# Performance work log

Hardware: AMD Instinct MI355X
Metric: run time of the kernel (lower is better)

## Reference

```python
import jax, jax.numpy as jnp
import numpy as np

# --- SLAYER params (nmnistNet.yaml) ---
THETA = 10.0
TS = 1.0
TAU_REF = 1.0
SCALE_REF = 2.0
T_SAMPLE = 300
B = 8

def _alpha_kernel(tau, mult, t_sample, ts, eps=0.01):
    vals = []
    t = 0.0
    while t < t_sample:
        v = mult * t / tau * np.exp(1.0 - t / tau)
        if abs(v) < eps and t > tau:
            break
        vals.append(v)
        t += ts
    return np.asarray(vals, np.float32)

# refractory kernel: alpha kernel with mult = -scaleRef*theta (slayer._calculateRefKernel)
REF_KERNEL = _alpha_kernel(TAU_REF, -SCALE_REF * THETA, T_SAMPLE, TS)
NREF = REF_KERNEL.shape[0]  # 11 for these params; REF_KERNEL[0] == 0


def spike(u):
    """slayerCuda.getSpikes: per-neuron sequential threshold recurrence over time.
    u: [..., T] membrane potential. On spike at t, REF_KERNEL is accumulated
    into u[t:t+NREF]; spike amplitude is 1/Ts."""
    uT = jnp.moveaxis(u, -1, 0)  # [T, ...]
    refk = jnp.asarray(REF_KERNEL[1:]).reshape((NREF - 1,) + (1,) * (u.ndim - 1))
    buf0 = jnp.zeros((NREF - 1,) + uT.shape[1:], u.dtype)  # pending refractory

    def step(buf, u_t):
        u_mod = u_t + buf[0]
        ev = (u_mod >= THETA).astype(u.dtype)
        buf = jnp.concatenate([buf[1:], jnp.zeros_like(buf[:1])], axis=0) + ev[None] * refk
        return buf, ev / TS

    _, s = jax.lax.scan(step, buf0, uT)
    return jnp.moveaxis(s, 0, -1)


def conv2d_t(x, w, pad):
    """slayer.conv: Conv3d with kernel (k,k,1) == per-timestep 2D conv.
    x: [B,C,H,W,T], w: [O,I,kh,kw]."""
    b, c, h, wd, t = x.shape
    xb = jnp.moveaxis(x, -1, 1).reshape(b * t, c, h, wd)
    y = jax.lax.conv_general_dilated(xb, w, (1, 1), [(pad, pad), (pad, pad)],
                                     dimension_numbers=('NCHW', 'OIHW', 'NCHW'))
    o, ho, wo = y.shape[1], y.shape[2], y.shape[3]
    return jnp.moveaxis(y.reshape(b, t, o, ho, wo), 1, -1)


def sum_pool2(x):
    """slayer.pool(2): fixed-weight (1.1*theta) 2x2/stride-2 sum over H,W per channel."""
    y = jax.lax.reduce_window(x, 0.0, jax.lax.add, (1, 1, 2, 2, 1), (1, 1, 2, 2, 1), 'VALID')
    return 1.1 * THETA * y


def setup_inputs():
    key = jax.random.key(0)
    k0, k1, k2, k3, k4 = jax.random.split(key, 5)
    spikeInput = (jax.random.uniform(k0, (B, 2, 34, 34, T_SAMPLE)) < 0.1).astype(jnp.float32) / TS
    # conv weights: kaiming-uniform bound * 100 (the __init__ scales conv weights by 100)
    w1 = jax.random.uniform(k1, (16, 2, 5, 5), minval=-14.1, maxval=14.1, dtype=jnp.float32)
    w2 = jax.random.uniform(k2, (32, 16, 3, 3), minval=-8.3, maxval=8.3, dtype=jnp.float32)
    w3 = jax.random.uniform(k3, (64, 32, 3, 3), minval=-5.9, maxval=5.9, dtype=jnp.float32)
    wfc = jax.random.uniform(k4, (10, 64, 8, 8), minval=-0.5, maxval=0.5, dtype=jnp.float32)
    return {"spikeInput": spikeInput, "w1": w1, "w2": w2, "w3": w3, "wfc": wfc}


def reference(spikeInput, w1, w2, w3, wfc):
    s1 = spike(conv2d_t(spikeInput, w1, 1))  # [B,16,32,32,T]
    s2 = spike(sum_pool2(s1))                # [B,16,16,16,T]
    s3 = spike(conv2d_t(s2, w2, 1))          # [B,32,16,16,T]
    s4 = spike(sum_pool2(s3))                # [B,32,8,8,T]
    s5 = spike(conv2d_t(s4, w3, 1))          # [B,64,8,8,T]
    # dense((8,8,64),10): Conv3d(64,10,(8,8,1)) == full-spatial contraction
    u = jnp.einsum('bchwt,ochw->bot', s5, wfc)[:, :, None, None, :]
    return spike(u)                          # [B,10,1,1,T]
```

## Files before the change

kernel.cpp:

```cpp
#include <hip/hip_runtime.h>
#include <hip/hip_bf16.h>
#include <cmath>

#define T_SAMPLE 300
#define NCHUNK 75

typedef __attribute__((ext_vector_type(8))) short short8;
typedef __attribute__((ext_vector_type(4))) float f32x4;

struct RefK { float v[10]; };

__device__ __forceinline__ unsigned char spike_step(float u, float* buf, const RefK& rk) {
    const float um = u + buf[0];
    const bool fire = um >= 10.0f;
    const float ev = fire ? 1.0f : 0.0f;
#pragma unroll
    for (int r = 0; r < 9; ++r) buf[r] = fmaf(ev, rk.v[r], buf[r + 1]);
    buf[9] = ev * rk.v[9];
    return fire ? (unsigned char)1 : (unsigned char)0;
}

__device__ __forceinline__ short8 bytes_to_bf16x8(uint2 w8) {
    union { uint4 u; short8 s8; } cv;
    cv.u.x = (w8.x & 0xFFu) * 0x3F80u | ((((w8.x >> 8) & 0xFFu) * 0x3F80u) << 16);
    cv.u.y = ((w8.x >> 16) & 0xFFu) * 0x3F80u | ((((w8.x >> 24) & 0xFFu) * 0x3F80u) << 16);
    cv.u.z = (w8.y & 0xFFu) * 0x3F80u | ((((w8.y >> 8) & 0xFFu) * 0x3F80u) << 16);
    cv.u.w = ((w8.y >> 16) & 0xFFu) * 0x3F80u | ((((w8.y >> 24) & 0xFFu) * 0x3F80u) << 16);
    return cv.s8;
}

__device__ __forceinline__ unsigned short bf16_split_sel(float w, int s) {
    __hip_bfloat16 hb = __float2bfloat16(w);
    const float hf = __bfloat162float(hb);
    __hip_bfloat16 mb = __float2bfloat16(w - hf);
    const float mf = __bfloat162float(mb);
    __hip_bfloat16 lb = __float2bfloat16(w - hf - mf);
    __hip_bfloat16 sel = (s == 0) ? hb : ((s == 1) ? mb : lb);
    return *(unsigned short*)&sel;
}

__global__ __launch_bounds__(256) void transpose_in_k(
    const float* __restrict__ In, unsigned int* __restrict__ X)
{
    __shared__ unsigned int lds[16 * NCHUNK];
    const int blk = blockIdx.x;
    const int tn = threadIdx.x >> 4;
    const int tq = threadIdx.x & 15;
    const size_t n = (size_t)blk * 16 + tn;
#pragma unroll
    for (int p = 0; p < 5; ++p) {
        const int ch = p * 16 + tq;
        if (ch < NCHUNK) {
            const float4 v = *(const float4*)(In + n * T_SAMPLE + ch * 4);
            unsigned int u = (v.x != 0.f ? 1u : 0u) | (v.y != 0.f ? 0x100u : 0u) |
                             (v.z != 0.f ? 0x10000u : 0u) | (v.w != 0.f ? 0x1000000u : 0u);
            lds[tn * NCHUNK + ch] = u;
        }
    }
    __syncthreads();
    for (int idx = threadIdx.x; idx < 16 * NCHUNK; idx += 256) {
        const int ch = idx >> 4, t2 = idx & 15;
        X[(size_t)ch * 18496 + blk * 16 + t2] = lds[t2 * NCHUNK + ch];
    }
}

__global__ __launch_bounds__(256) void prep_w1_k(
    const float* __restrict__ w1, unsigned short* __restrict__ Wr1)
{
    const int g = blockIdx.x * 256 + threadIdx.x;
    const int j = g & 7;
    const int lane = (g >> 3) & 63;
    const int ks = (g >> 9) & 3;
    const int s = g >> 11;
    const int q = lane >> 4;
    const int oc = lane & 15;
    const int kg = ks * 32 + q * 8 + j;
    const int slot = kg >> 2, c = kg & 1;
    const int dy = slot / 6, dx = slot % 6;
    const float w = (dy < 5 && dx < 5) ? w1[((oc * 2 + c) * 5 + dy) * 5 + dx] * 0.5f : 0.f;
    Wr1[g] = bf16_split_sel(w, s);
}

__global__ __launch_bounds__(256) void prep_w3_k(
    const float* __restrict__ w3, unsigned short* __restrict__ Wr)
{
    const int g = blockIdx.x * 256 + threadIdx.x;
    const int j = g & 7;
    const int lane = (g >> 3) & 63;
    const int mt = (g >> 9) & 3;
    const int rest = g >> 11;
    const int ks = rest % 9;
    const int s = rest / 9;
    const int oc = mt * 16 + (lane & 15);
    const int ic = (lane >> 4) * 8 + j;
    Wr[g] = bf16_split_sel(w3[(oc * 32 + ic) * 9 + ks], s);
}

__global__ __launch_bounds__(256) void prep_w2_k(
    const float* __restrict__ w2, unsigned short* __restrict__ Wr2)
{
    const int g = blockIdx.x * 256 + threadIdx.x;
    const int j = g & 7;
    const int lane = (g >> 3) & 63;
    const int mt = (g >> 9) & 1;
    const int rest = g >> 10;
    const int kp = rest % 5;
    const int s = rest / 5;
    const int q = lane >> 4;
    const int oc = mt * 16 + (lane & 15);
    const int tap = kp * 2 + (q >> 1);
    const int ic = (q & 1) * 8 + j;
    const float w = (tap <= 8) ? w2[(oc * 16 + ic) * 9 + tap] : 0.f;
    Wr2[g] = bf16_split_sel(w, s);
}

__device__ __forceinline__ void c1_mfma_chunk(
    const unsigned int* __restrict__ tb, const int* offA, const int* offB,
    const short8* Af, f32x4* acc)
{
    unsigned int vA[4][4], vB[4][4];
#pragma unroll
    for (int ks = 0; ks < 4; ++ks)
#pragma unroll
        for (int t = 0; t < 4; ++t) {
            vA[ks][t] = tb[t * 72 + offA[ks]];
            vB[ks][t] = tb[t * 72 + offB[ks]];
        }

#pragma unroll
    for (int t = 0; t < 4; ++t) acc[t] = (f32x4){0.f, 0.f, 0.f, 0.f};
#pragma unroll
    for (int ks = 0; ks < 4; ++ks)
#pragma unroll
        for (int t = 0; t < 4; ++t) {
            union { uint4 u; short8 s8; } cv;
            cv.u.x = vA[ks][t]; cv.u.y = vA[ks][t];
            cv.u.z = vB[ks][t]; cv.u.w = vB[ks][t];
#pragma unroll
            for (int s = 0; s < 3; ++s)
                acc[t] = __builtin_amdgcn_mfma_f32_16x16x32_bf16(
                    Af[s * 4 + ks], cv.s8, acc[t], 0, 0, 0);
        }
}

__global__ __launch_bounds__(256) void conv1ps_k(
    const unsigned int* __restrict__ X, const unsigned short* __restrict__ Wr1,
    uchar4* __restrict__ S1, RefK rk)
{
    __shared__ unsigned int tab[15 * 288];
    __shared__ __align__(16) float4 Ulds[15 * 256];
    const int pg = blockIdx.x;
    const int b = blockIdx.y;
    const int ty = pg >> 2, tx = pg & 3;
    const int tid = threadIdx.x;
    const int wv = tid >> 6, lane = tid & 63;
    const int q = lane >> 4, n = lane & 15;
    const int py0 = n >> 3, px0 = n & 7;

    short8 Af[12];
#pragma unroll
    for (int s = 0; s < 3; ++s)
#pragma unroll
        for (int ks = 0; ks < 4; ++ks)
            Af[s * 4 + ks] = *(const short8*)(Wr1 + (((s * 4 + ks) * 64 + lane) * 8));

    int offA[4], offB[4];
#pragma unroll
    for (int ks = 0; ks < 4; ++ks) {
        const int sA = ks * 8 + q * 2, sB = sA + 1;
        const int dyA = sA / 6, dxA = sA - dyA * 6;
        const int dyB = sB / 6, dxB = sB - dyB * 6;
        offA[ks] = min(py0 + dyA, 5) * 12 + min(px0 + dxA, 11);
        offB[ks] = min(py0 + dyB, 5) * 12 + min(px0 + dxB, 11);
    }

    int lidx[5];
    int gof[5];
#pragma unroll
    for (int i = 0; i < 5; ++i) {
        const int e = i * 256 + tid;
        if (e < 1080) {
            const int chl = e / 72, site = e - chl * 72;
            const int r = site / 12, cc = site - r * 12;
            const int gy = ty * 2 - 1 + r, gx = tx * 8 - 1 + cc;
            lidx[i] = chl * 288 + site;
            gof[i] = (((unsigned)gy < 34u) && ((unsigned)gx < 34u))
                   ? (chl * 18496 + (b * 2) * 1156 + gy * 34 + gx) : -1;
        } else { lidx[i] = -1; gof[i] = -1; }
    }

    unsigned int w0[5], w1[5];
#pragma unroll
    for (int i = 0; i < 5; ++i) {
        if (gof[i] >= 0) { w0[i] = X[gof[i]]; w1[i] = X[gof[i] + 1156]; }
        else { w0[i] = 0u; w1[i] = 0u; }
    }

    float buf[10];
#pragma unroll
    for (int r = 0; r < 10; ++r) buf[r] = 0.f;
    const int s_oc = tid >> 4, s_n = tid & 15;
    const int nb0 = (b * 16 + s_oc) * 1024 + (ty * 2 + (s_n >> 3)) * 32 + tx * 8 + (s_n & 7);

    for (int w = 0; w < 5; ++w) {
#pragma unroll
        for (int i = 0; i < 5; ++i) {
            if (lidx[i] >= 0) {
#pragma unroll
                for (int t = 0; t < 4; ++t)
                    tab[lidx[i] + t * 72] =
                        ((w0[i] >> (8 * t)) & 0xFFu) * 0x3F80u
                        | ((((w1[i] >> (8 * t)) & 0xFFu) * 0x3F80u) << 16);
            }
        }
        __syncthreads();

        for (int k = wv; k < 15; k += 4) {
            f32x4 acc[4];
            c1_mfma_chunk(tab + k * 288, offA, offB, Af, acc);
#pragma unroll
            for (int rr = 0; rr < 4; ++rr)
                Ulds[k * 256 + (q * 4 + rr) * 16 + n] =
                    make_float4(acc[0][rr], acc[1][rr], acc[2][rr], acc[3][rr]);
        }
        __syncthreads();

        if (w < 4) {
            const unsigned int* Xs = X + (size_t)(w + 1) * (15 * 18496);
#pragma unroll
            for (int i = 0; i < 5; ++i) {
                if (gof[i] >= 0) { w0[i] = Xs[gof[i]]; w1[i] = Xs[gof[i] + 1156]; }
            }
        }

        for (int k = 0; k < 15; ++k) {
            const float4 u = Ulds[k * 256 + tid];
            uchar4 o;
            o.x = spike_step(u.x, buf, rk);
            o.y = spike_step(u.y, buf, rk);
            o.z = spike_step(u.z, buf, rk);
            o.w = spike_step(u.w, buf, rk);
            S1[(size_t)(w * 15 + k) * 131072 + nb0] = o;
        }
    }
}

__global__ __launch_bounds__(256) void conv2_mfma_k(
    const unsigned int* __restrict__ s2u, const unsigned short* __restrict__ Wr2,
    float4* __restrict__ U, int b0, int nbl)
{
    __shared__ __align__(16) unsigned char pad[4 * 18 * 18 * 16];
    const int tc = blockIdx.x;
    const int bl = blockIdx.z;
    const int b = b0 + bl;
    const int tid = threadIdx.x;
    const int wv = tid >> 6, lane = tid & 63;
    const int q = lane >> 4, n = lane & 15;
    const int PLANE_U = nbl * 8192;

    unsigned int* lp = (unsigned int*)pad;
    for (int i = tid; i < 5184; i += 256) lp[i] = 0u;
    __syncthreads();
    const unsigned int* sb = s2u + (size_t)tc * 32768 + b * 4096;
    for (int e = tid; e < 4096; e += 256) {
        const unsigned int v = sb[e];
        const int c = e >> 8, pix = e & 255;
        const int base = (((pix >> 4) + 1) * 18 + ((pix & 15) + 1)) * 16 + c;
        pad[base]         = (unsigned char)(v & 0xFFu);
        pad[5184 + base]  = (unsigned char)((v >> 8) & 0xFFu);
        pad[10368 + base] = (unsigned char)((v >> 16) & 0xFFu);
        pad[15552 + base] = (unsigned char)(v >> 24);
    }
    __syncthreads();

    for (int i = 0; i < 4; ++i) {
        const int r = wv * 4 + i;
        f32x4 acc[2][4];
#pragma unroll
        for (int mt = 0; mt < 2; ++mt)
#pragma unroll
            for (int t = 0; t < 4; ++t) acc[mt][t] = (f32x4){0.f, 0.f, 0.f, 0.f};

        for (int kp = 0; kp < 5; ++kp) {
            short8 Af[6];
#pragma unroll
            for (int s = 0; s < 3; ++s)
#pragma unroll
                for (int mt = 0; mt < 2; ++mt)
                    Af[s * 2 + mt] = *(const short8*)(Wr2 + ((((s * 5 + kp) * 2 + mt) * 64 + lane) * 8));
            int tap = kp * 2 + (q >> 1);
            if (tap > 8) tap = 8;
            const int dy = tap / 3, dx = tap % 3;
#pragma unroll
            for (int t = 0; t < 4; ++t) {
                const int off = ((t * 18 + r + dy) * 18 + (n + dx)) * 16 + (q & 1) * 8;
                const short8 Bf = bytes_to_bf16x8(*(const uint2*)(pad + off));
#pragma unroll
                for (int s = 0; s < 3; ++s)
#pragma unroll
                    for (int mt = 0; mt < 2; ++mt)
                        acc[mt][t] = __builtin_amdgcn_mfma_f32_16x16x32_bf16(
                            Af[s * 2 + mt], Bf, acc[mt][t], 0, 0, 0);
            }
        }

        const size_t ub = (size_t)tc * PLANE_U;
#pragma unroll
        for (int mt = 0; mt < 2; ++mt)
#pragma unroll
            for (int rr = 0; rr < 4; ++rr) {
                const int oc = mt * 16 + q * 4 + rr;
                const int nb = (bl * 32 + oc) * 256 + r * 16 + n;
                U[ub + nb] = make_float4(acc[mt][0][rr], acc[mt][1][rr], acc[mt][2][rr], acc[mt][3][rr]);
            }
    }
}

__global__ __launch_bounds__(256) void conv3_mfma_k(
    const unsigned int* __restrict__ s4u, const unsigned short* __restrict__ Wr,
    float4* __restrict__ U)
{
    __shared__ __align__(16) unsigned char pad[12800];
    const int tc = blockIdx.x;
    const int bl = blockIdx.z;
    const int tid = threadIdx.x;
    const int wv = tid >> 6, lane = tid & 63;
    const int q = lane >> 4, n = lane & 15;

    unsigned int* lp = (unsigned int*)pad;
    for (int i = tid; i < 3200; i += 256) lp[i] = 0u;
    __syncthreads();
    const unsigned int* sb = s4u + (size_t)tc * 16384 + bl * 2048;
    for (int e = tid; e < 2048; e += 256) {
        const unsigned int v = sb[e];
        const int c = e >> 6, pix = e & 63;
        const int base = (((pix >> 3) + 1) * 10 + ((pix & 7) + 1)) * 32 + c;
        pad[base]        = (unsigned char)(v & 0xFFu);
        pad[3200 + base] = (unsigned char)((v >> 8) & 0xFFu);
        pad[6400 + base] = (unsigned char)((v >> 16) & 0xFFu);
        pad[9600 + base] = (unsigned char)(v >> 24);
    }
    __syncthreads();

    const int pixel = wv * 16 + n;
    const int py0 = pixel >> 3, px0 = pixel & 7;

    f32x4 acc[4][4];
#pragma unroll
    for (int mt = 0; mt < 4; ++mt)
#pragma unroll
        for (int t = 0; t < 4; ++t) acc[mt][t] = (f32x4){0.f, 0.f, 0.f, 0.f};

    for (int ks = 0; ks < 9; ++ks) {
        const int dy = ks / 3, dx = ks % 3;
        short8 Af[12];
#pragma unroll
        for (int s = 0; s < 3; ++s)
#pragma unroll
            for (int mt = 0; mt < 4; ++mt)
                Af[s * 4 + mt] = *(const short8*)(Wr + ((((s * 9 + ks) * 4 + mt) * 64 + lane) * 8));
#pragma unroll
        for (int t = 0; t < 4; ++t) {
            const int off = ((t * 10 + py0 + dy) * 10 + (px0 + dx)) * 32 + q * 8;
            const short8 Bf = bytes_to_bf16x8(*(const uint2*)(pad + off));
#pragma unroll
            for (int s = 0; s < 3; ++s)
#pragma unroll
                for (int mt = 0; mt < 4; ++mt)
                    acc[mt][t] = __builtin_amdgcn_mfma_f32_16x16x32_bf16(
                        Af[s * 4 + mt], Bf, acc[mt][t], 0, 0, 0);
        }
    }

    const size_t ub = (size_t)tc * 32768 + (size_t)bl * 4096;
#pragma unroll
    for (int mt = 0; mt < 4; ++mt)
#pragma unroll
        for (int r = 0; r < 4; ++r) {
            const int oc = mt * 16 + q * 4 + r;
            const int nb = oc * 64 + wv * 16 + n;
            U[ub + nb] = make_float4(acc[mt][0][r], acc[mt][1][r], acc[mt][2][r], acc[mt][3][r]);
        }
}

__device__ __forceinline__ void spike_body(
    const float4* __restrict__ U, uchar4* __restrict__ S,
    int nneur, int sstride, int soff, const RefK& rk)
{
    const int n = blockIdx.x * 64 + threadIdx.x;
    const float4* up = U + n;
    uchar4* sp = S + soff + n;
    float buf[10];
#pragma unroll
    for (int r = 0; r < 10; ++r) buf[r] = 0.f;

    float4 ring[8];
#pragma unroll
    for (int r = 0; r < 8; ++r) ring[r] = up[(size_t)r * nneur];

#pragma unroll 8
    for (int ch = 0; ch < 72; ++ch) {
        const float4 cur = ring[ch & 7];
        const int pf = (ch + 8 < NCHUNK) ? ch + 8 : NCHUNK - 1;
        ring[ch & 7] = up[(size_t)pf * nneur];
        uchar4 o;
        o.x = spike_step(cur.x, buf, rk);
        o.y = spike_step(cur.y, buf, rk);
        o.z = spike_step(cur.z, buf, rk);
        o.w = spike_step(cur.w, buf, rk);
        sp[(size_t)ch * sstride] = o;
    }
#pragma unroll
    for (int ch = 72; ch < NCHUNK; ++ch) {
        const float4 cur = ring[ch & 7];
        uchar4 o;
        o.x = spike_step(cur.x, buf, rk);
        o.y = spike_step(cur.y, buf, rk);
        o.z = spike_step(cur.z, buf, rk);
        o.w = spike_step(cur.w, buf, rk);
        sp[(size_t)ch * sstride] = o;
    }
}

__global__ __launch_bounds__(64) void spike2_k(
    const float4* U, uchar4* S, int nneur, int sstride, int soff, RefK rk)
{ spike_body(U, S, nneur, sstride, soff, rk); }

__global__ __launch_bounds__(64) void spike3_k(
    const float4* U, uchar4* S, int nneur, int sstride, int soff, RefK rk)
{ spike_body(U, S, nneur, sstride, soff, rk); }

__device__ __forceinline__ int bsum4(uint2 r0, uint2 r1, int k) {
    return (int)((r0.x >> (8 * k)) & 0xffu) + (int)((r0.y >> (8 * k)) & 0xffu)
         + (int)((r1.x >> (8 * k)) & 0xffu) + (int)((r1.y >> (8 * k)) & 0xffu);
}

template <int C, int H, int W>
__device__ __forceinline__ void pool_body(
    const uchar4* __restrict__ Sin, uchar4* __restrict__ Sout, const RefK& rk)
{
    constexpr int H2 = H / 2, W2 = W / 2;
    constexpr int SIN = 8 * C * H * W;
    constexpr int SOUT = 8 * C * H2 * W2;
    const int n = blockIdx.x * 64 + threadIdx.x;
    const int x = n % W2;
    const int y = (n / W2) % H2;
    const int c = (n / (W2 * H2)) % C;
    const int b = n / (W2 * H2 * C);
    const int base = (((b * C + c) * H + 2 * y) * W + 2 * x);
    uchar4* q = Sout + n;

    float buf[10];
#pragma unroll
    for (int r = 0; r < 10; ++r) buf[r] = 0.f;

    uint2 r0[8], r1[8];
#pragma unroll
    for (int r = 0; r < 8; ++r) {
        r0[r] = *(const uint2*)(Sin + (size_t)r * SIN + base);
        r1[r] = *(const uint2*)(Sin + (size_t)r * SIN + base + W);
    }

#pragma unroll 8
    for (int ch = 0; ch < 72; ++ch) {
        const uint2 a0 = r0[ch & 7], a1 = r1[ch & 7];
        const int pf = (ch + 8 < NCHUNK) ? ch + 8 : NCHUNK - 1;
        r0[ch & 7] = *(const uint2*)(Sin + (size_t)pf * SIN + base);
        r1[ch & 7] = *(const uint2*)(Sin + (size_t)pf * SIN + base + W);
        uchar4 o;
        o.x = spike_step(11.0f * (float)bsum4(a0, a1, 0), buf, rk);
        o.y = spike_step(11.0f * (float)bsum4(a0, a1, 1), buf, rk);
        o.z = spike_step(11.0f * (float)bsum4(a0, a1, 2), buf, rk);
        o.w = spike_step(11.0f * (float)bsum4(a0, a1, 3), buf, rk);
        q[(size_t)ch * SOUT] = o;
    }
#pragma unroll
    for (int ch = 72; ch < NCHUNK; ++ch) {
        const uint2 a0 = r0[ch & 7], a1 = r1[ch & 7];
        uchar4 o;
        o.x = spike_step(11.0f * (float)bsum4(a0, a1, 0), buf, rk);
        o.y = spike_step(11.0f * (float)bsum4(a0, a1, 1), buf, rk);
        o.z = spike_step(11.0f * (float)bsum4(a0, a1, 2), buf, rk);
        o.w = spike_step(11.0f * (float)bsum4(a0, a1, 3), buf, rk);
        q[(size_t)ch * SOUT] = o;
    }
}

__global__ __launch_bounds__(64) void pool2_k(
    const uchar4* Sin, uchar4* Sout, RefK rk) { pool_body<16, 32, 32>(Sin, Sout, rk); }
__global__ __launch_bounds__(64) void pool4_k(
    const uchar4* Sin, uchar4* Sout, RefK rk) { pool_body<32, 16, 16>(Sin, Sout, rk); }

__global__ __launch_bounds__(64) void dense_k(
    const uchar4* __restrict__ S5, const float* __restrict__ WFC,
    float4* __restrict__ U6)
{
    const int tc = blockIdx.x, o = blockIdx.y, b = blockIdx.z;
    const int lane = threadIdx.x;
    float a0 = 0.f, a1 = 0.f, a2 = 0.f, a3 = 0.f;
    const uchar4* sb = S5 + (size_t)tc * 32768 + b * 4096;
    const float* wb = WFC + o * 4096;
    for (int i = 0; i < 64; ++i) {
        const int site = i * 64 + lane;
        const uchar4 s = sb[site];
        const float w = wb[site];
        a0 = fmaf(w, (float)s.x, a0);
        a1 = fmaf(w, (float)s.y, a1);
        a2 = fmaf(w, (float)s.z, a2);
        a3 = fmaf(w, (float)s.w, a3);
    }
#pragma unroll
    for (int m = 1; m < 64; m <<= 1) {
        a0 += __shfl_xor(a0, m, 64);
        a1 += __shfl_xor(a1, m, 64);
        a2 += __shfl_xor(a2, m, 64);
        a3 += __shfl_xor(a3, m, 64);
    }
    if (lane == 0)
        U6[(size_t)tc * 80 + b * 10 + o] = make_float4(a0, a1, a2, a3);
}

__global__ __launch_bounds__(128) void spike6_k(
    const float4* __restrict__ U6, float* __restrict__ Out, RefK rk)
{
    const int n = threadIdx.x;
    if (n >= 80) return;
    const float4* up = U6 + n;
    float* op = Out + (size_t)n * T_SAMPLE;
    float buf[10];
#pragma unroll
    for (int r = 0; r < 10; ++r) buf[r] = 0.f;

    float4 ring[8];
#pragma unroll
    for (int r = 0; r < 8; ++r) ring[r] = up[(size_t)r * 80];

#pragma unroll 8
    for (int ch = 0; ch < 72; ++ch) {
        const float4 cur = ring[ch & 7];
        const int pf = (ch + 8 < NCHUNK) ? ch + 8 : NCHUNK - 1;
        ring[ch & 7] = up[(size_t)pf * 80];
        float4 o;
        o.x = (float)spike_step(cur.x, buf, rk);
        o.y = (float)spike_step(cur.y, buf, rk);
        o.z = (float)spike_step(cur.z, buf, rk);
        o.w = (float)spike_step(cur.w, buf, rk);
        *(float4*)(op + ch * 4) = o;
    }
#pragma unroll
    for (int ch = 72; ch < NCHUNK; ++ch) {
        const float4 cur = ring[ch & 7];
        float4 o;
        o.x = (float)spike_step(cur.x, buf, rk);
        o.y = (float)spike_step(cur.y, buf, rk);
        o.z = (float)spike_step(cur.z, buf, rk);
        o.w = (float)spike_step(cur.w, buf, rk);
        *(float4*)(op + ch * 4) = o;
    }
}

extern "C" void kernel_launch(void* const* d_in, const int* in_sizes, int n_in,
                              void* d_out, int out_size, void* d_ws, size_t ws_size,
                              hipStream_t stream)
{
    const float* spikeIn = (const float*)d_in[0];
    const float* w1 = (const float*)d_in[1];
    const float* w2 = (const float*)d_in[2];
    const float* w3 = (const float*)d_in[3];
    const float* wfc = (const float*)d_in[4];
    float* out = (float*)d_out;

    RefK rk;
    for (int t = 1; t <= 10; ++t)
        rk.v[t - 1] = (float)(-20.0 * (double)t * std::exp(1.0 - (double)t));

    const size_t A_BYTES = 39321600;
    const size_t B_BYTES = 9830400;
    const size_t U6_BYTES = 96000;
    const size_t U_BIG = 78643200, U_SMALL = 39321600;
    const size_t TAIL = A_BYTES + B_BYTES + U6_BYTES;
    const bool big = ws_size >= U_BIG + TAIL;
    const size_t U_BYTES = big ? U_BIG : U_SMALL;

    char* ws = (char*)d_ws;
    float4* U = (float4*)ws;
    uchar4* A = (uchar4*)(ws + U_BYTES);
    uchar4* Bb = (uchar4*)(ws + U_BYTES + A_BYTES);
    float4* U6 = (float4*)(ws + U_BYTES + A_BYTES + B_BYTES);
    unsigned short* Wr = (unsigned short*)(ws + U_BYTES + 20971520);
    unsigned short* Wr2 = (unsigned short*)(ws + U_BYTES + 20971520 + 131072);
    unsigned short* Wr1 = (unsigned short*)(ws + U_BYTES + A_BYTES + 5570560);

    uchar4* X = Bb;
    uchar4* s1 = A;
    uchar4* s2 = Bb;
    uchar4* s3 = A;
    uchar4* s4 = Bb;
    uchar4* s5 = A;

    transpose_in_k<<<18496 / 16, 256, 0, stream>>>(spikeIn, (unsigned int*)X);
    prep_w1_k<<<24, 256, 0, stream>>>(w1, Wr1);

    {
        dim3 g1(64, 8);
        conv1ps_k<<<g1, 256, 0, stream>>>((const unsigned int*)X, Wr1, s1, rk);
    }
    pool2_k<<<32768 / 64, 64, 0, stream>>>(s1, s2, rk);
    prep_w2_k<<<60, 256, 0, stream>>>(w2, Wr2);
    prep_w3_k<<<216, 256, 0, stream>>>(w3, Wr);
    const int nbl2 = big ? 8 : 4;
    for (int b0 = 0; b0 < 8; b0 += nbl2) {
        dim3 g2(NCHUNK, 1, nbl2);
        conv2_mfma_k<<<g2, 256, 0, stream>>>((const unsigned int*)s2, Wr2, U, b0, nbl2);
        const int nn = nbl2 * 8192;
        spike2_k<<<nn / 64, 64, 0, stream>>>(U, s3, nn, 65536, b0 * 8192, rk);
    }
    pool4_k<<<16384 / 64, 64, 0, stream>>>(s3, s4, rk);
    {
        dim3 g3(NCHUNK, 1, 8);
        conv3_mfma_k<<<g3, 256, 0, stream>>>((const unsigned int*)s4, Wr, U);
        spike3_k<<<32768 / 64, 64, 0, stream>>>(U, s5, 32768, 32768, 0, rk);
    }
    dim3 g6(NCHUNK, 10, 8);
    dense_k<<<g6, 64, 0, stream>>>(s5, wfc, U6);
    spike6_k<<<1, 128, 0, stream>>>(U6, out, rk);
}
```

Measured before the change: 259.3 us.

## Warp-specialize conv1 into producer/consumer waves and fuse dense outputs per block

Conv1 now launches 512-thread blocks. Four waves compute MFMA convolution chunks into double-buffered LDS while the other four run the sequential spike recurrence on the previous chunk, so compute and the serial threshold scan overlap. The input loads for the next window are also prefetched into a second tab buffer. Separately, dense_k computes all 10 outputs in one block instead of one block per output, reusing each spike load across outputs at the cost of many more registers.

```diff
diff --git a/kernel.cpp b/kernel.cpp
--- a/kernel.cpp
+++ b/kernel.cpp
@@ -143,104 +143,130 @@
         }
 }
 
-__global__ __launch_bounds__(256) void conv1ps_k(
+__global__ __launch_bounds__(512, 4) void conv1pc_k(
     const unsigned int* __restrict__ X, const unsigned short* __restrict__ Wr1,
     uchar4* __restrict__ S1, RefK rk)
 {
-    __shared__ unsigned int tab[15 * 288];
-    __shared__ __align__(16) float4 Ulds[15 * 256];
+    __shared__ unsigned int tab[2][5 * 288];
+    __shared__ __align__(16) float4 Ulds[2][5 * 256];
     const int pg = blockIdx.x;
     const int b = blockIdx.y;
     const int ty = pg >> 2, tx = pg & 3;
     const int tid = threadIdx.x;
     const int wv = tid >> 6, lane = tid & 63;
+    const bool isConv = (wv >= 4);
     const int q = lane >> 4, n = lane & 15;
     const int py0 = n >> 3, px0 = n & 7;
 
     short8 Af[12];
-#pragma unroll
-    for (int s = 0; s < 3; ++s)
-#pragma unroll
-        for (int ks = 0; ks < 4; ++ks)
-            Af[s * 4 + ks] = *(const short8*)(Wr1 + (((s * 4 + ks) * 64 + lane) * 8));
-
     int offA[4], offB[4];
-#pragma unroll
-    for (int ks = 0; ks < 4; ++ks) {
-        const int sA = ks * 8 + q * 2, sB = sA + 1;
-        const int dyA = sA / 6, dxA = sA - dyA * 6;
-        const int dyB = sB / 6, dxB = sB - dyB * 6;
-        offA[ks] = min(py0 + dyA, 5) * 12 + min(px0 + dxA, 11);
-        offB[ks] = min(py0 + dyB, 5) * 12 + min(px0 + dxB, 11);
-    }
-
-    int lidx[5];
-    int gof[5];
-#pragma unroll
-    for (int i = 0; i < 5; ++i) {
-        const int e = i * 256 + tid;
-        if (e < 1080) {
-            const int chl = e / 72, site = e - chl * 72;
-            const int r = site / 12, cc = site - r * 12;
-            const int gy = ty * 2 - 1 + r, gx = tx * 8 - 1 + cc;
-            lidx[i] = chl * 288 + site;
-            gof[i] = (((unsigned)gy < 34u) && ((unsigned)gx < 34u))
-                   ? (chl * 18496 + (b * 2) * 1156 + gy * 34 + gx) : -1;
-        } else { lidx[i] = -1; gof[i] = -1; }
-    }
-
-    unsigned int w0[5], w1[5];
-#pragma unroll
-    for (int i = 0; i < 5; ++i) {
-        if (gof[i] >= 0) { w0[i] = X[gof[i]]; w1[i] = X[gof[i] + 1156]; }
-        else { w0[i] = 0u; w1[i] = 0u; }
-    }
-
-    float buf[10];
-#pragma unroll
-    for (int r = 0; r < 10; ++r) buf[r] = 0.f;
-    const int s_oc = tid >> 4, s_n = tid & 15;
-    const int nb0 = (b * 16 + s_oc) * 1024 + (ty * 2 + (s_n >> 3)) * 32 + tx * 8 + (s_n & 7);
-
-    for (int w = 0; w < 5; ++w) {
-#pragma unroll
-        for (int i = 0; i < 5; ++i) {
+    int lidx[2], gof[2];
+    unsigned int w0[2], w1[2];
+    if (isConv) {
+#pragma unroll
+        for (int s = 0; s < 3; ++s)
+#pragma unroll
+            for (int ks = 0; ks < 4; ++ks)
+                Af[s * 4 + ks] = *(const short8*)(Wr1 + (((s * 4 + ks) * 64 + lane) * 8));
+#pragma unroll
+        for (int ks = 0; ks < 4; ++ks) {
+            const int sA = ks * 8 + q * 2, sB = sA + 1;
+            const int dyA = sA / 6, dxA = sA - dyA * 6;
+            const int dyB = sB / 6, dxB = sB - dyB * 6;
+            offA[ks] = min(py0 + dyA, 5) * 12 + min(px0 + dxA, 11);
+            offB[ks] = min(py0 + dyB, 5) * 12 + min(px0 + dxB, 11);
+        }
+        const int tid2 = tid - 256;
+#pragma unroll
+        for (int i = 0; i < 2; ++i) {
+            const int e = i * 256 + tid2;
+            if (e < 360) {
+                const int chl = e / 72, site = e - chl * 72;
+                const int r = site / 12, cc = site - r * 12;
+                const int gy = ty * 2 - 1 + r, gx = tx * 8 - 1 + cc;
+                lidx[i] = chl * 288 + site;
+                gof[i] = (((unsigned)gy < 34u) && ((unsigned)gx < 34u))
+                       ? (chl * 18496 + (b * 2) * 1156 + gy * 34 + gx) : -1;
+            } else { lidx[i] = -1; gof[i] = -1; }
+        }
+#pragma unroll
+        for (int i = 0; i < 2; ++i) {
+            if (gof[i] >= 0) { w0[i] = X[gof[i]]; w1[i] = X[gof[i] + 1156]; }
+            else { w0[i] = 0u; w1[i] = 0u; }
+        }
+#pragma unroll
+        for (int i = 0; i < 2; ++i) {
             if (lidx[i] >= 0) {
 #pragma unroll
                 for (int t = 0; t < 4; ++t)
-                    tab[lidx[i] + t * 72] =
+                    tab[0][lidx[i] + t * 72] =
                         ((w0[i] >> (8 * t)) & 0xFFu) * 0x3F80u
                         | ((((w1[i] >> (8 * t)) & 0xFFu) * 0x3F80u) << 16);
             }
         }
+    }
+
+    float buf[10];
+#pragma unroll
+    for (int r = 0; r < 10; ++r) buf[r] = 0.f;
+    const int s_oc = (tid & 255) >> 4, s_n = tid & 15;
+    const int nb0 = (b * 16 + s_oc) * 1024 + (ty * 2 + (s_n >> 3)) * 32 + tx * 8 + (s_n & 7);
+
+    __syncthreads();
+
+    for (int w = 0; w < 15; ++w) {
+        const int cb = w & 1;
+        if (isConv) {
+            if (w < 14) {
+                const unsigned int* Xs = X + (size_t)(w + 1) * (5 * 18496);
+#pragma unroll
+                for (int i = 0; i < 2; ++i) {
+                    if (gof[i] >= 0) { w0[i] = Xs[gof[i]]; w1[i] = Xs[gof[i] + 1156]; }
+                }
+            }
+            for (int k = wv - 4; k < 5; k += 4) {
+                f32x4 acc[4];
+                c1_mfma_chunk(&tab[cb][k * 288], offA, offB, Af, acc);
+#pragma unroll
+                for (int rr = 0; rr < 4; ++rr)
+                    Ulds[cb][k * 256 + (q * 4 + rr) * 16 + n] =
+                        make_float4(acc[0][rr], acc[1][rr], acc[2][rr], acc[3][rr]);
+            }
+            if (w < 14) {
+#pragma unroll
+                for (int i = 0; i < 2; ++i) {
+                    if (lidx[i] >= 0) {
+#pragma unroll
+                        for (int t = 0; t < 4; ++t)
+                            tab[cb ^ 1][lidx[i] + t * 72] =
+                                ((w0[i] >> (8 * t)) & 0xFFu) * 0x3F80u
+                                | ((((w1[i] >> (8 * t)) & 0xFFu) * 0x3F80u) << 16);
+                    }
+                }
+            }
+        } else if (w > 0) {
+            const int pb = (w - 1) & 1;
+            for (int k = 0; k < 5; ++k) {
+                const float4 u = Ulds[pb][k * 256 + tid];
+                uchar4 o;
+                o.x = spike_step(u.x, buf, rk);
+                o.y = spike_step(u.y, buf, rk);
+                o.z = spike_step(u.z, buf, rk);
+                o.w = spike_step(u.w, buf, rk);
+                S1[(size_t)((w - 1) * 5 + k) * 131072 + nb0] = o;
+            }
+        }
         __syncthreads();
-
-        for (int k = wv; k < 15; k += 4) {
-            f32x4 acc[4];
-            c1_mfma_chunk(tab + k * 288, offA, offB, Af, acc);
-#pragma unroll
-            for (int rr = 0; rr < 4; ++rr)
-                Ulds[k * 256 + (q * 4 + rr) * 16 + n] =
-                    make_float4(acc[0][rr], acc[1][rr], acc[2][rr], acc[3][rr]);
-        }
-        __syncthreads();
-
-        if (w < 4) {
-            const unsigned int* Xs = X + (size_t)(w + 1) * (15 * 18496);
-#pragma unroll
-            for (int i = 0; i < 5; ++i) {
-                if (gof[i] >= 0) { w0[i] = Xs[gof[i]]; w1[i] = Xs[gof[i] + 1156]; }
-            }
-        }
-
-        for (int k = 0; k < 15; ++k) {
-            const float4 u = Ulds[k * 256 + tid];
+    }
+    if (!isConv) {
+        for (int k = 0; k < 5; ++k) {
+            const float4 u = Ulds[0][k * 256 + tid];
             uchar4 o;
             o.x = spike_step(u.x, buf, rk);
             o.y = spike_step(u.y, buf, rk);
             o.z = spike_step(u.z, buf, rk);
             o.w = spike_step(u.w, buf, rk);
-            S1[(size_t)(w * 15 + k) * 131072 + nb0] = o;
+            S1[(size_t)(70 + k) * 131072 + nb0] = o;
         }
     }
 }
@@ -495,29 +521,45 @@
     const uchar4* __restrict__ S5, const float* __restrict__ WFC,
     float4* __restrict__ U6)
 {
-    const int tc = blockIdx.x, o = blockIdx.y, b = blockIdx.z;
+    const int tc = blockIdx.x, b = blockIdx.z;
     const int lane = threadIdx.x;
-    float a0 = 0.f, a1 = 0.f, a2 = 0.f, a3 = 0.f;
+    float a[10][4];
+#pragma unroll
+    for (int o = 0; o < 10; ++o)
+#pragma unroll
+        for (int j = 0; j < 4; ++j) a[o][j] = 0.f;
+
     const uchar4* sb = S5 + (size_t)tc * 32768 + b * 4096;
-    const float* wb = WFC + o * 4096;
+#pragma unroll 4
     for (int i = 0; i < 64; ++i) {
         const int site = i * 64 + lane;
         const uchar4 s = sb[site];
-        const float w = wb[site];
-        a0 = fmaf(w, (float)s.x, a0);
-        a1 = fmaf(w, (float)s.y, a1);
-        a2 = fmaf(w, (float)s.z, a2);
-        a3 = fmaf(w, (float)s.w, a3);
-    }
-#pragma unroll
-    for (int m = 1; m < 64; m <<= 1) {
-        a0 += __shfl_xor(a0, m, 64);
-        a1 += __shfl_xor(a1, m, 64);
-        a2 += __shfl_xor(a2, m, 64);
-        a3 += __shfl_xor(a3, m, 64);
-    }
-    if (lane == 0)
-        U6[(size_t)tc * 80 + b * 10 + o] = make_float4(a0, a1, a2, a3);
+        const float sx = (float)s.x, sy = (float)s.y;
+        const float sz = (float)s.z, sw = (float)s.w;
+#pragma unroll
+        for (int o = 0; o < 10; ++o) {
+            const float w = WFC[o * 4096 + site];
+            a[o][0] = fmaf(w, sx, a[o][0]);
+            a[o][1] = fmaf(w, sy, a[o][1]);
+            a[o][2] = fmaf(w, sz, a[o][2]);
+            a[o][3] = fmaf(w, sw, a[o][3]);
+        }
+    }
+#pragma unroll
+    for (int o = 0; o < 10; ++o)
+#pragma unroll
+        for (int m = 1; m < 64; m <<= 1) {
+            a[o][0] += __shfl_xor(a[o][0], m, 64);
+            a[o][1] += __shfl_xor(a[o][1], m, 64);
+            a[o][2] += __shfl_xor(a[o][2], m, 64);
+            a[o][3] += __shfl_xor(a[o][3], m, 64);
+        }
+    if (lane == 0) {
+#pragma unroll
+        for (int o = 0; o < 10; ++o)
+            U6[(size_t)tc * 80 + b * 10 + o] =
+                make_float4(a[o][0], a[o][1], a[o][2], a[o][3]);
+    }
 }
 
 __global__ __launch_bounds__(128) void spike6_k(
@@ -603,7 +645,7 @@
 
     {
         dim3 g1(64, 8);
-        conv1ps_k<<<g1, 256, 0, stream>>>((const unsigned int*)X, Wr1, s1, rk);
+        conv1pc_k<<<g1, 512, 0, stream>>>((const unsigned int*)X, Wr1, s1, rk);
     }
     pool2_k<<<32768 / 64, 64, 0, stream>>>(s1, s2, rk);
     prep_w2_k<<<60, 256, 0, stream>>>(w2, Wr2);
@@ -621,7 +663,9 @@
         conv3_mfma_k<<<g3, 256, 0, stream>>>((const unsigned int*)s4, Wr, U);
         spike3_k<<<32768 / 64, 64, 0, stream>>>(U, s5, 32768, 32768, 0, rk);
     }
-    dim3 g6(NCHUNK, 10, 8);
-    dense_k<<<g6, 64, 0, stream>>>(s5, wfc, U6);
+    {
+        dim3 g6(NCHUNK, 1, 8);
+        dense_k<<<g6, 64, 0, stream>>>(s5, wfc, U6);
+    }
     spike6_k<<<1, 128, 0, stream>>>(U6, out, rk);
 }
```

New measurement: 272.3 us. +5.0%, slower.
